# Kernel optimization log

Hardware: AMD Instinct MI355X
Metric: run time of the kernel (lower is better)

The kernel has to match this reference:

```python
import jax, jax.numpy as jnp
import numpy as np

LN_EPS = 1e-5
N, D = 512, 512


def setup_inputs() -> dict:
    key = jax.random.key(0)
    ks = jax.random.split(key, 3)
    s1 = 1.0 / np.sqrt(2 * D)  # torch Linear default-ish scale
    s2 = 1.0 / np.sqrt(D)
    return {
        "embeddings": jax.random.normal(ks[0], (N, D), jnp.float32),
        "W1": jax.random.normal(ks[1], (2 * D, D), jnp.float32) * s1,  # [in, out]
        "b1": jnp.zeros((D,), jnp.float32),
        "gamma": jnp.ones((D,), jnp.float32),
        "beta": jnp.zeros((D,), jnp.float32),
        "W2": jax.random.normal(ks[2], (D, 1), jnp.float32) * s2,
        "b2": jnp.zeros((1,), jnp.float32),
    }


def reference(embeddings, W1, b1, gamma, beta, W2, b2):
    d = embeddings.shape[-1]
    # Linear(2D -> D) on cat(e_i, e_j) decomposes into two GEMMs + broadcast add,
    # avoiding materializing the [N, N, 2D] concatenated pair tensor.
    left = embeddings @ W1[:d]              # [N, D]  (contribution of e_i)
    right = embeddings @ W1[d:] + b1        # [N, D]  (contribution of e_j + bias)
    h = left[:, None, :] + right[None, :, :]  # [N, N, D]
    # LayerNorm over last dim (eps matches torch default)
    mu = h.mean(axis=-1, keepdims=True)
    var = ((h - mu) ** 2).mean(axis=-1, keepdims=True)
    h = (h - mu) * jax.lax.rsqrt(var + LN_EPS) * gamma + beta
    # exact GELU (torch nn.GELU default)
    h = jax.nn.gelu(h, approximate=False)
    s = jax.nn.sigmoid(jnp.squeeze(h @ W2, -1) + b2[0])  # [N, N]
    # original loop only evaluates pairs i <= j and mirrors to (j, i)
    n = s.shape[0]
    upper = jnp.arange(n)[:, None] <= jnp.arange(n)[None, :]
    return jnp.where(upper, s, s.T)
```

## Files before the change

kernel.cpp:

```cpp
#include <hip/hip_runtime.h>


#define N_ 512
#define D_ 512

__global__ __launch_bounds__(512, 2) void k_gemm(const float* __restrict__ E,
                                                 const float* __restrict__ W1,
                                                 const float* __restrict__ b1,
                                                 float* __restrict__ W ) {
    __shared__ float et[512 * 20];

    const int t = threadIdx.x;
    const int bg = blockIdx.x;
    const int rg = bg >> 4;
    const int cg = bg & 15;
    const int r0 = rg * 16;
    const int half = cg >> 3;
    const int cb = (cg & 7) << 6;

    for (int x = t; x < 16 * 128; x += 512) {
        const int r = x >> 7, k4 = (x & 127) << 2;
        float4 v = *(const float4*)&E[(r0 + r) * D_ + k4];
        et[(k4 + 0) * 20 + r] = v.x;
        et[(k4 + 1) * 20 + r] = v.y;
        et[(k4 + 2) * 20 + r] = v.z;
        et[(k4 + 3) * 20 + r] = v.w;
    }
    __syncthreads();

    const int lane = t & 63;
    const int ks = t >> 6;
    const int kb = ks << 6;
    const int c4 = (lane & 15) << 2;
    const int rq = ((lane >> 4) & 3) << 2;
    const float* __restrict__ wp = W1 + (half << 18) + (kb << 9) + cb + c4;

    float4 a0 = {0.f, 0.f, 0.f, 0.f}, a1 = {0.f, 0.f, 0.f, 0.f};
    float4 a2 = {0.f, 0.f, 0.f, 0.f}, a3 = {0.f, 0.f, 0.f, 0.f};
#pragma unroll 4
    for (int k = 0; k < 64; ++k) {
        float4 wv = *(const float4*)(wp + (k << 9));
        float4 ev = *(const float4*)&et[(kb + k) * 20 + rq];
        a0.x = fmaf(ev.x, wv.x, a0.x); a0.y = fmaf(ev.x, wv.y, a0.y);
        a0.z = fmaf(ev.x, wv.z, a0.z); a0.w = fmaf(ev.x, wv.w, a0.w);
        a1.x = fmaf(ev.y, wv.x, a1.x); a1.y = fmaf(ev.y, wv.y, a1.y);
        a1.z = fmaf(ev.y, wv.z, a1.z); a1.w = fmaf(ev.y, wv.w, a1.w);
        a2.x = fmaf(ev.z, wv.x, a2.x); a2.y = fmaf(ev.z, wv.y, a2.y);
        a2.z = fmaf(ev.z, wv.z, a2.z); a2.w = fmaf(ev.z, wv.w, a2.w);
        a3.x = fmaf(ev.w, wv.x, a3.x); a3.y = fmaf(ev.w, wv.y, a3.y);
        a3.z = fmaf(ev.w, wv.z, a3.z); a3.w = fmaf(ev.w, wv.w, a3.w);
    }

    __syncthreads();
    float* red = et;
    const int ob = (ks << 10) + c4;
    *(float4*)&red[ob + ((rq + 0) << 6)] = a0;
    *(float4*)&red[ob + ((rq + 1) << 6)] = a1;
    *(float4*)&red[ob + ((rq + 2) << 6)] = a2;
    *(float4*)&red[ob + ((rq + 3) << 6)] = a3;
    __syncthreads();

    float2 s = {0.f, 0.f};
#pragma unroll
    for (int k2 = 0; k2 < 8; ++k2) {
        float2 p = *(const float2*)&red[(k2 << 10) + (t << 1)];
        s.x += p.x; s.y += p.y;
    }
    const int ro = t >> 5, co = (t << 1) & 63;
    if (half) {
        float2 bb = *(const float2*)&b1[cb + co];
        s.x += bb.x; s.y += bb.y;
    }
    *(float2*)&W[((half << 9) + r0 + ro) * D_ + cb + co] = s;
}


#define GELU1(L, R, G, BE, WC, RST, T2N, ACC)                                 \
    do {                                                                      \
        float s_ = (L) + (R);                                                 \
        float x_ = fmaf(fmaf(s_, (RST), (T2N)), (G), (BE));                   \
        float q_ = x_ * fmaf(-0.10294340f, x_ * x_, -2.30220935f);            \
        float e_ = __builtin_amdgcn_exp2f(q_);                                \
        float ge_ = x_ * __builtin_amdgcn_rcpf(1.f + e_);                     \
        ACC = fmaf(ge_, (WC), ACC);                                           \
    } while (0)

#define GELU4(LQ, RQ, RST, T2N, ACC)                                          \
    do {                                                                      \
        GELU1(LQ.x, RQ.x, g4.x, be4.x, w4.x, RST, T2N, ACC);                  \
        GELU1(LQ.y, RQ.y, g4.y, be4.y, w4.y, RST, T2N, ACC);                  \
        GELU1(LQ.z, RQ.z, g4.z, be4.z, w4.z, RST, T2N, ACC);                  \
        GELU1(LQ.w, RQ.w, g4.w, be4.w, w4.w, RST, T2N, ACC);                  \
    } while (0)

#define DOT4(LQ, RQ, ACC)                                                     \
    ACC += LQ.x * RQ.x + LQ.y * RQ.y + LQ.z * RQ.z + LQ.w * RQ.w

#define BFLY(V)                                                               \
    do {                                                                      \
        V += __shfl_xor(V, 1, 64);                                            \
        V += __shfl_xor(V, 2, 64);                                            \
        V += __shfl_xor(V, 4, 64);                                            \
        V += __shfl_xor(V, 8, 64);                                            \
    } while (0)

__global__ __launch_bounds__(512, 2) void k_pair(const float* __restrict__ W,
                                                 const float* __restrict__ gf,
                                                 const float* __restrict__ bef,
                                                 const float* __restrict__ wf,
                                                 const float* __restrict__ b2f,
                                                 float* __restrict__ out) {
    __shared__ float ls[16][516];
    __shared__ float rs[16][516];
    __shared__ float smean[32];
    __shared__ float svar[32];

    const int b = blockIdx.x;
    int I = (int)((65.0f - sqrtf(4225.0f - 8.0f * (float)b)) * 0.5f);
    if (I < 0) I = 0;
    if (I > 31) I = 31;
#define S_(i) (32 * (i) - ((i) * ((i)-1)) / 2)
    while (S_(I) > b) --I;
    while (S_(I + 1) <= b) ++I;
    const int J = I + (b - S_(I));
#undef S_

    const int t = threadIdx.x;
    const int ks = t & 15;
    const int pt = t >> 4;
    const int i2 = (pt & 7) * 2, j4 = (pt >> 3) * 4;
    const int Ibase = I * 16, Jbase = N_ + J * 16;

    for (int x = t; x < 16 * 128; x += 512) {
        int r = x >> 7, c4 = (x & 127) << 2;
        *(float4*)&ls[r][c4] = *(const float4*)&W[(Ibase + r) * D_ + c4];
        *(float4*)&rs[r][c4] = *(const float4*)&W[(Jbase + r) * D_ + c4];
    }
    __syncthreads();

    {
        const int lane = t & 63, w = t >> 6;
#pragma unroll
        for (int rr = 0; rr < 4; ++rr) {
            const int row = w * 4 + rr;
            const float* p = (row < 16) ? &ls[row][0] : &rs[row - 16][0];
            float4 a = *(const float4*)&p[lane << 2];
            float4 c = *(const float4*)&p[256 + (lane << 2)];
            float sm = (a.x + a.y) + (a.z + a.w) + (c.x + c.y) + (c.z + c.w);
            float sq = a.x * a.x + a.y * a.y + a.z * a.z + a.w * a.w +
                       c.x * c.x + c.y * c.y + c.z * c.z + c.w * c.w;
#pragma unroll
            for (int off = 32; off > 0; off >>= 1) {
                sm += __shfl_xor(sm, off, 64);
                sq += __shfl_xor(sq, off, 64);
            }
            if (lane == 0) {
                float mu = sm * (1.f / D_);
                smean[row] = mu;
                svar[row] = fmaf(-mu, mu, sq * (1.f / D_));
            }
        }
    }
    __syncthreads();

    float cv0 = 0.f, cv1 = 0.f, cv2 = 0.f, cv3 = 0.f;
    float cv4 = 0.f, cv5 = 0.f, cv6 = 0.f, cv7 = 0.f;
    for (int it = 0; it < 8; ++it) {
        const int kq = (it * 16 + ks) * 4;
        float4 la = *(float4*)&ls[i2][kq];
        float4 lb = *(float4*)&ls[i2 + 1][kq];
        float4 ra = *(float4*)&rs[j4][kq];
        float4 rb = *(float4*)&rs[j4 + 1][kq];
        float4 rc = *(float4*)&rs[j4 + 2][kq];
        float4 rd = *(float4*)&rs[j4 + 3][kq];
        DOT4(la, ra, cv0); DOT4(la, rb, cv1); DOT4(la, rc, cv2); DOT4(la, rd, cv3);
        DOT4(lb, ra, cv4); DOT4(lb, rb, cv5); DOT4(lb, rc, cv6); DOT4(lb, rd, cv7);
    }
    BFLY(cv0); BFLY(cv1); BFLY(cv2); BFLY(cv3);
    BFLY(cv4); BFLY(cv5); BFLY(cv6); BFLY(cv7);

    const float ml0 = smean[i2], ml1 = smean[i2 + 1];
    const float vl0 = svar[i2], vl1 = svar[i2 + 1];
    const float mr0 = smean[16 + j4],     mr1 = smean[16 + j4 + 1];
    const float mr2 = smean[16 + j4 + 2], mr3 = smean[16 + j4 + 3];
    const float vr0 = svar[16 + j4],     vr1 = svar[16 + j4 + 1];
    const float vr2 = svar[16 + j4 + 2], vr3 = svar[16 + j4 + 3];
    const float rst0 = rsqrtf(vl0 + vr0 + cv0 * (2.f / D_) - 2.f * ml0 * mr0 + 1e-5f);
    const float rst1 = rsqrtf(vl0 + vr1 + cv1 * (2.f / D_) - 2.f * ml0 * mr1 + 1e-5f);
    const float rst2 = rsqrtf(vl0 + vr2 + cv2 * (2.f / D_) - 2.f * ml0 * mr2 + 1e-5f);
    const float rst3 = rsqrtf(vl0 + vr3 + cv3 * (2.f / D_) - 2.f * ml0 * mr3 + 1e-5f);
    const float rst4 = rsqrtf(vl1 + vr0 + cv4 * (2.f / D_) - 2.f * ml1 * mr0 + 1e-5f);
    const float rst5 = rsqrtf(vl1 + vr1 + cv5 * (2.f / D_) - 2.f * ml1 * mr1 + 1e-5f);
    const float rst6 = rsqrtf(vl1 + vr2 + cv6 * (2.f / D_) - 2.f * ml1 * mr2 + 1e-5f);
    const float rst7 = rsqrtf(vl1 + vr3 + cv7 * (2.f / D_) - 2.f * ml1 * mr3 + 1e-5f);
    const float t2n0 = -(ml0 + mr0) * rst0;
    const float t2n1 = -(ml0 + mr1) * rst1;
    const float t2n2 = -(ml0 + mr2) * rst2;
    const float t2n3 = -(ml0 + mr3) * rst3;
    const float t2n4 = -(ml1 + mr0) * rst4;
    const float t2n5 = -(ml1 + mr1) * rst5;
    const float t2n6 = -(ml1 + mr2) * rst6;
    const float t2n7 = -(ml1 + mr3) * rst7;

    float ac0 = 0.f, ac1 = 0.f, ac2 = 0.f, ac3 = 0.f;
    float ac4 = 0.f, ac5 = 0.f, ac6 = 0.f, ac7 = 0.f;
    for (int it = 0; it < 8; ++it) {
        const int kq = (it * 16 + ks) * 4;
        float4 g4 = *(const float4*)&gf[kq];
        float4 be4 = *(const float4*)&bef[kq];
        float4 w4 = *(const float4*)&wf[kq];
        float4 la = *(float4*)&ls[i2][kq];
        float4 lb = *(float4*)&ls[i2 + 1][kq];
        float4 ra = *(float4*)&rs[j4][kq];
        float4 rb = *(float4*)&rs[j4 + 1][kq];
        float4 rc = *(float4*)&rs[j4 + 2][kq];
        float4 rd = *(float4*)&rs[j4 + 3][kq];
        GELU4(la, ra, rst0, t2n0, ac0); GELU4(la, rb, rst1, t2n1, ac1);
        GELU4(la, rc, rst2, t2n2, ac2); GELU4(la, rd, rst3, t2n3, ac3);
        GELU4(lb, ra, rst4, t2n4, ac4); GELU4(lb, rb, rst5, t2n5, ac5);
        GELU4(lb, rc, rst6, t2n6, ac6); GELU4(lb, rd, rst7, t2n7, ac7);
    }
    BFLY(ac0); BFLY(ac1); BFLY(ac2); BFLY(ac3);
    BFLY(ac4); BFLY(ac5); BFLY(ac6); BFLY(ac7);

    if (ks == 0) {
        const float bb = b2f[0];
        const float z0 = __builtin_amdgcn_rcpf(
            1.f + __builtin_amdgcn_exp2f(-1.44269504f * (ac0 + bb)));
        const float z1 = __builtin_amdgcn_rcpf(
            1.f + __builtin_amdgcn_exp2f(-1.44269504f * (ac1 + bb)));
        const float z2 = __builtin_amdgcn_rcpf(
            1.f + __builtin_amdgcn_exp2f(-1.44269504f * (ac2 + bb)));
        const float z3 = __builtin_amdgcn_rcpf(
            1.f + __builtin_amdgcn_exp2f(-1.44269504f * (ac3 + bb)));
        const float z4 = __builtin_amdgcn_rcpf(
            1.f + __builtin_amdgcn_exp2f(-1.44269504f * (ac4 + bb)));
        const float z5 = __builtin_amdgcn_rcpf(
            1.f + __builtin_amdgcn_exp2f(-1.44269504f * (ac5 + bb)));
        const float z6 = __builtin_amdgcn_rcpf(
            1.f + __builtin_amdgcn_exp2f(-1.44269504f * (ac6 + bb)));
        const float z7 = __builtin_amdgcn_rcpf(
            1.f + __builtin_amdgcn_exp2f(-1.44269504f * (ac7 + bb)));
        const int gi0 = Ibase + i2;
        const int gj0 = (Jbase - N_) + j4;
        if (I < J) {
            float4 o0 = {z0, z1, z2, z3};
            float4 o1 = {z4, z5, z6, z7};
            *(float4*)&out[gi0 * N_ + gj0] = o0;
            *(float4*)&out[(gi0 + 1) * N_ + gj0] = o1;
            out[gj0 * N_ + gi0] = z0;       out[gj0 * N_ + gi0 + 1] = z4;
            out[(gj0 + 1) * N_ + gi0] = z1; out[(gj0 + 1) * N_ + gi0 + 1] = z5;
            out[(gj0 + 2) * N_ + gi0] = z2; out[(gj0 + 2) * N_ + gi0 + 1] = z6;
            out[(gj0 + 3) * N_ + gi0] = z3; out[(gj0 + 3) * N_ + gi0 + 1] = z7;
        } else {
            if (gi0 <= gj0)     { out[gi0 * N_ + gj0] = z0;       out[gj0 * N_ + gi0] = z0; }
            if (gi0 <= gj0 + 1) { out[gi0 * N_ + gj0 + 1] = z1;   out[(gj0 + 1) * N_ + gi0] = z1; }
            if (gi0 <= gj0 + 2) { out[gi0 * N_ + gj0 + 2] = z2;   out[(gj0 + 2) * N_ + gi0] = z2; }
            if (gi0 <= gj0 + 3) { out[gi0 * N_ + gj0 + 3] = z3;   out[(gj0 + 3) * N_ + gi0] = z3; }
            if (gi0 + 1 <= gj0)     { out[(gi0 + 1) * N_ + gj0] = z4;     out[gj0 * N_ + gi0 + 1] = z4; }
            if (gi0 + 1 <= gj0 + 1) { out[(gi0 + 1) * N_ + gj0 + 1] = z5; out[(gj0 + 1) * N_ + gi0 + 1] = z5; }
            if (gi0 + 1 <= gj0 + 2) { out[(gi0 + 1) * N_ + gj0 + 2] = z6; out[(gj0 + 2) * N_ + gi0 + 1] = z6; }
            if (gi0 + 1 <= gj0 + 3) { out[(gi0 + 1) * N_ + gj0 + 3] = z7; out[(gj0 + 3) * N_ + gi0 + 1] = z7; }
        }
    }
}

extern "C" void kernel_launch(void* const* d_in, const int* in_sizes, int n_in,
                              void* d_out, int out_size, void* d_ws, size_t ws_size,
                              hipStream_t stream) {
    const float* E     = (const float*)d_in[0];
    const float* W1    = (const float*)d_in[1];
    const float* b1    = (const float*)d_in[2];
    const float* gamma = (const float*)d_in[3];
    const float* beta  = (const float*)d_in[4];
    const float* w2    = (const float*)d_in[5];
    const float* b2    = (const float*)d_in[6];
    float* out = (float*)d_out;

    float* lcrc = (float*)d_ws;

    k_gemm<<<512, 512, 0, stream>>>(E, W1, b1, lcrc);
    k_pair<<<528, 512, 0, stream>>>(lcrc, gamma, beta, w2, b2, out);
}
```

Measured before the change: 123.2 us.

## Split pair tiles to 16x8 blocks of 256 threads, keep left rows in registers

Result: slower. 140.6 us (+14.2%).

```diff
diff --git a/kernel.cpp b/kernel.cpp
--- a/kernel.cpp
+++ b/kernel.cpp
@@ -37,7 +37,7 @@
 
     float4 a0 = {0.f, 0.f, 0.f, 0.f}, a1 = {0.f, 0.f, 0.f, 0.f};
     float4 a2 = {0.f, 0.f, 0.f, 0.f}, a3 = {0.f, 0.f, 0.f, 0.f};
-#pragma unroll 4
+#pragma unroll 8
     for (int k = 0; k < 64; ++k) {
         float4 wv = *(const float4*)(wp + (k << 9));
         float4 ev = *(const float4*)&et[(kb + k) * 20 + rq];
@@ -104,45 +104,79 @@
         V += __shfl_xor(V, 8, 64);                                            \
     } while (0)
 
-__global__ __launch_bounds__(512, 2) void k_pair(const float* __restrict__ W,
+#define PASSA(IT, LA, LB)                                                     \
+    do {                                                                      \
+        const int kq = ((IT)*16 + ks) * 4;                                    \
+        LA = *(float4*)&ls[i2][kq];                                           \
+        LB = *(float4*)&ls[i2 + 1][kq];                                       \
+        float4 ra = *(float4*)&rs[j4][kq];                                    \
+        float4 rb = *(float4*)&rs[j4 + 1][kq];                                \
+        float4 rc = *(float4*)&rs[j4 + 2][kq];                                \
+        float4 rd = *(float4*)&rs[j4 + 3][kq];                                \
+        DOT4(LA, ra, cv0); DOT4(LA, rb, cv1);                                 \
+        DOT4(LA, rc, cv2); DOT4(LA, rd, cv3);                                 \
+        DOT4(LB, ra, cv4); DOT4(LB, rb, cv5);                                 \
+        DOT4(LB, rc, cv6); DOT4(LB, rd, cv7);                                 \
+    } while (0)
+
+#define PASSB(IT, LA, LB)                                                     \
+    do {                                                                      \
+        const int kq = ((IT)*16 + ks) * 4;                                    \
+        float4 g4 = *(const float4*)&gf[kq];                                  \
+        float4 be4 = *(const float4*)&bef[kq];                                \
+        float4 w4 = *(const float4*)&wf[kq];                                  \
+        float4 ra = *(float4*)&rs[j4][kq];                                    \
+        float4 rb = *(float4*)&rs[j4 + 1][kq];                                \
+        float4 rc = *(float4*)&rs[j4 + 2][kq];                                \
+        float4 rd = *(float4*)&rs[j4 + 3][kq];                                \
+        GELU4(LA, ra, rst0, t2n0, ac0); GELU4(LA, rb, rst1, t2n1, ac1);       \
+        GELU4(LA, rc, rst2, t2n2, ac2); GELU4(LA, rd, rst3, t2n3, ac3);       \
+        GELU4(LB, ra, rst4, t2n4, ac4); GELU4(LB, rb, rst5, t2n5, ac5);       \
+        GELU4(LB, rc, rst6, t2n6, ac6); GELU4(LB, rd, rst7, t2n7, ac7);       \
+    } while (0)
+
+__global__ __launch_bounds__(256, 3) void k_pair(const float* __restrict__ W,
                                                  const float* __restrict__ gf,
                                                  const float* __restrict__ bef,
                                                  const float* __restrict__ wf,
                                                  const float* __restrict__ b2f,
                                                  float* __restrict__ out) {
     __shared__ float ls[16][516];
-    __shared__ float rs[16][516];
-    __shared__ float smean[32];
-    __shared__ float svar[32];
+    __shared__ float rs[8][516];
+    __shared__ float smean[24];
+    __shared__ float svar[24];
 
     const int b = blockIdx.x;
-    int I = (int)((65.0f - sqrtf(4225.0f - 8.0f * (float)b)) * 0.5f);
+    int I = (int)((65.0f - sqrtf(4225.0f - 4.0f * (float)b)) * 0.5f);
     if (I < 0) I = 0;
     if (I > 31) I = 31;
-#define S_(i) (32 * (i) - ((i) * ((i)-1)) / 2)
+#define S_(i) (65 * (i) - (i) * (i))
     while (S_(I) > b) --I;
     while (S_(I + 1) <= b) ++I;
-    const int J = I + (b - S_(I));
+    const int J = 2 * I + (b - S_(I));
 #undef S_
 
     const int t = threadIdx.x;
     const int ks = t & 15;
     const int pt = t >> 4;
-    const int i2 = (pt & 7) * 2, j4 = (pt >> 3) * 4;
-    const int Ibase = I * 16, Jbase = N_ + J * 16;
-
-    for (int x = t; x < 16 * 128; x += 512) {
+    const int i2 = (pt & 7) * 2;
+    const int j4 = (pt >> 3) * 4;
+    const int Ibase = I * 16, Jbase = N_ + J * 8;
+
+    for (int x = t; x < 24 * 128; x += 256) {
         int r = x >> 7, c4 = (x & 127) << 2;
-        *(float4*)&ls[r][c4] = *(const float4*)&W[(Ibase + r) * D_ + c4];
-        *(float4*)&rs[r][c4] = *(const float4*)&W[(Jbase + r) * D_ + c4];
+        if (r < 16)
+            *(float4*)&ls[r][c4] = *(const float4*)&W[(Ibase + r) * D_ + c4];
+        else
+            *(float4*)&rs[r - 16][c4] = *(const float4*)&W[(Jbase + r - 16) * D_ + c4];
     }
     __syncthreads();
 
     {
         const int lane = t & 63, w = t >> 6;
 #pragma unroll
-        for (int rr = 0; rr < 4; ++rr) {
-            const int row = w * 4 + rr;
+        for (int rr = 0; rr < 6; ++rr) {
+            const int row = w * 6 + rr;
             const float* p = (row < 16) ? &ls[row][0] : &rs[row - 16][0];
             float4 a = *(const float4*)&p[lane << 2];
             float4 c = *(const float4*)&p[256 + (lane << 2)];
@@ -165,17 +199,10 @@
 
     float cv0 = 0.f, cv1 = 0.f, cv2 = 0.f, cv3 = 0.f;
     float cv4 = 0.f, cv5 = 0.f, cv6 = 0.f, cv7 = 0.f;
-    for (int it = 0; it < 8; ++it) {
-        const int kq = (it * 16 + ks) * 4;
-        float4 la = *(float4*)&ls[i2][kq];
-        float4 lb = *(float4*)&ls[i2 + 1][kq];
-        float4 ra = *(float4*)&rs[j4][kq];
-        float4 rb = *(float4*)&rs[j4 + 1][kq];
-        float4 rc = *(float4*)&rs[j4 + 2][kq];
-        float4 rd = *(float4*)&rs[j4 + 3][kq];
-        DOT4(la, ra, cv0); DOT4(la, rb, cv1); DOT4(la, rc, cv2); DOT4(la, rd, cv3);
-        DOT4(lb, ra, cv4); DOT4(lb, rb, cv5); DOT4(lb, rc, cv6); DOT4(lb, rd, cv7);
-    }
+    float4 la0, la1, la2, la3, la4, la5, la6, la7;
+    float4 lb0, lb1, lb2, lb3, lb4, lb5, lb6, lb7;
+    PASSA(0, la0, lb0); PASSA(1, la1, lb1); PASSA(2, la2, lb2); PASSA(3, la3, lb3);
+    PASSA(4, la4, lb4); PASSA(5, la5, lb5); PASSA(6, la6, lb6); PASSA(7, la7, lb7);
     BFLY(cv0); BFLY(cv1); BFLY(cv2); BFLY(cv3);
     BFLY(cv4); BFLY(cv5); BFLY(cv6); BFLY(cv7);
 
@@ -204,22 +231,8 @@
 
     float ac0 = 0.f, ac1 = 0.f, ac2 = 0.f, ac3 = 0.f;
     float ac4 = 0.f, ac5 = 0.f, ac6 = 0.f, ac7 = 0.f;
-    for (int it = 0; it < 8; ++it) {
-        const int kq = (it * 16 + ks) * 4;
-        float4 g4 = *(const float4*)&gf[kq];
-        float4 be4 = *(const float4*)&bef[kq];
-        float4 w4 = *(const float4*)&wf[kq];
-        float4 la = *(float4*)&ls[i2][kq];
-        float4 lb = *(float4*)&ls[i2 + 1][kq];
-        float4 ra = *(float4*)&rs[j4][kq];
-        float4 rb = *(float4*)&rs[j4 + 1][kq];
-        float4 rc = *(float4*)&rs[j4 + 2][kq];
-        float4 rd = *(float4*)&rs[j4 + 3][kq];
-        GELU4(la, ra, rst0, t2n0, ac0); GELU4(la, rb, rst1, t2n1, ac1);
-        GELU4(la, rc, rst2, t2n2, ac2); GELU4(la, rd, rst3, t2n3, ac3);
-        GELU4(lb, ra, rst4, t2n4, ac4); GELU4(lb, rb, rst5, t2n5, ac5);
-        GELU4(lb, rc, rst6, t2n6, ac6); GELU4(lb, rd, rst7, t2n7, ac7);
-    }
+    PASSB(0, la0, lb0); PASSB(1, la1, lb1); PASSB(2, la2, lb2); PASSB(3, la3, lb3);
+    PASSB(4, la4, lb4); PASSB(5, la5, lb5); PASSB(6, la6, lb6); PASSB(7, la7, lb7);
     BFLY(ac0); BFLY(ac1); BFLY(ac2); BFLY(ac3);
     BFLY(ac4); BFLY(ac5); BFLY(ac6); BFLY(ac7);
 
@@ -243,7 +256,7 @@
             1.f + __builtin_amdgcn_exp2f(-1.44269504f * (ac7 + bb)));
         const int gi0 = Ibase + i2;
         const int gj0 = (Jbase - N_) + j4;
-        if (I < J) {
+        if (J >= 2 * I + 2) {
             float4 o0 = {z0, z1, z2, z3};
             float4 o1 = {z4, z5, z6, z7};
             *(float4*)&out[gi0 * N_ + gj0] = o0;
@@ -280,5 +293,5 @@
     float* lcrc = (float*)d_ws;
 
     k_gemm<<<512, 512, 0, stream>>>(E, W1, b1, lcrc);
-    k_pair<<<528, 512, 0, stream>>>(lcrc, gamma, beta, w2, b2, out);
+    k_pair<<<1056, 256, 0, stream>>>(lcrc, gamma, beta, w2, b2, out);
 }
```
